# Optimization experiments

Measured on AMD Instinct MI355X. Metric: run time of the kernel, lower is better.

The kernel has to match this reference:

```python
import jax, jax.numpy as jnp
import numpy as np

B, C, H, W = 1, 96, 128, 128
P = 4            # patch_size
E = 192          # embed_dim
DI = 384         # d_inner = expand * embed_dim
NS = 16          # d_state
R = 12           # dt_rank = ceil(E/16)
K = 4            # scan directions
NBLK = 8         # SS2D_MBs_num
GW = C // 2      # SCPA group width


def layernorm(x, g, b, eps=1e-5):
    mu = x.mean(-1, keepdims=True)
    v = x.var(-1, keepdims=True)
    return (x - mu) * jax.lax.rsqrt(v + eps) * g + b


def batchnorm(x, g, b, m, v, eps=1e-5):
    # eval-mode BatchNorm2d over channel axis 1 of (B,C,H,W)
    return (x - m[:, None, None]) * jax.lax.rsqrt(v + eps)[:, None, None] * g[:, None, None] + b[:, None, None]


def conv2d(x, w):
    return jax.lax.conv_general_dilated(x, w, (1, 1), 'SAME', dimension_numbers=('NCHW', 'OIHW', 'NCHW'))


def dwconv2d(x, w, b):
    out = jax.lax.conv_general_dilated(x, w[:, None], (1, 1), 'SAME',
                                       dimension_numbers=('NCHW', 'OIHW', 'NCHW'),
                                       feature_group_count=w.shape[0])
    return out + b[None, :, None, None]


def lrelu(x):
    return jnp.where(x >= 0, x, 0.2 * x)


def channel_attention(x, w1, w2):
    # CBAM-style: shared MLP on avg+max pooled channel descriptors, sigmoid gate
    avg = x.mean((2, 3))
    mx = x.max((2, 3))
    mlp = lambda v: jax.nn.relu(v @ w1.T) @ w2.T
    attn = jax.nn.sigmoid(mlp(avg) + mlp(mx))
    return x * attn[:, :, None, None]


def selective_scan(xs, dts, A, Bs, Cs, Dskip):
    # xs,dts: (B,K,DI,L); A: (K,DI,NS); Bs,Cs: (B,K,NS,L); Dskip: (K,DI)
    xs_t = jnp.moveaxis(xs, -1, 0)
    dts_t = jnp.moveaxis(dts, -1, 0)
    Bs_t = jnp.moveaxis(Bs, -1, 0)
    Cs_t = jnp.moveaxis(Cs, -1, 0)
    h0 = jnp.zeros(xs.shape[:3] + (NS,), xs.dtype)  # (B,K,DI,NS)

    def step(h, t):
        xt, dt, Bt, Ct = t
        h = jnp.exp(dt[..., None] * A) * h + (dt * xt)[..., None] * Bt[:, :, None, :]
        return h, jnp.sum(h * Ct[:, :, None, :], axis=-1)

    _, ys = jax.lax.scan(step, h0, (xs_t, dts_t, Bs_t, Cs_t))
    return jnp.moveaxis(ys, 0, -1) + xs * Dskip[None, :, :, None]


def ss2d_block(x, p):
    # VMamba-style VSS block: x + SS2D(LN(x)); x: (B,Hp,Wp,E)
    (ln_g, ln_b, inproj_w, conv_w, conv_b, xproj_w, dtproj_w, dtproj_b,
     Alog, Dskip, on_g, on_b, outproj_w, merge_w) = p
    Bsz, Hp, Wp, _ = x.shape
    L = Hp * Wp
    h = layernorm(x, ln_g, ln_b)
    xz = jnp.einsum('bhwd,ed->bhwe', h, inproj_w)   # (B,Hp,Wp,2*DI)
    xc, z = jnp.split(xz, 2, axis=-1)
    xc = jax.nn.silu(dwconv2d(jnp.transpose(xc, (0, 3, 1, 2)), conv_w, conv_b))  # (B,DI,Hp,Wp)
    # 4-direction cross-scan: row-major, col-major and their reverses
    xf = xc.reshape(Bsz, DI, L)
    xwh = jnp.transpose(xc, (0, 1, 3, 2)).reshape(Bsz, DI, L)
    xs = jnp.stack([xf, xwh, jnp.flip(xf, -1), jnp.flip(xwh, -1)], axis=1)  # (B,K,DI,L)
    x_dbl = jnp.einsum('bkdl,kcd->bkcl', xs, xproj_w)  # (B,K,R+2*NS,L)
    dts, Bm, Cm = jnp.split(x_dbl, [R, R + NS], axis=2)
    dts = jax.nn.softplus(jnp.einsum('bkrl,kdr->bkdl', dts, dtproj_w) + dtproj_b[None, :, :, None])
    A = -jnp.exp(Alog)
    oy = selective_scan(xs, dts, A, Bm, Cm, Dskip)  # (B,K,DI,L)
    y0 = oy[:, 0]
    y1 = jnp.transpose(oy[:, 1].reshape(Bsz, DI, Wp, Hp), (0, 1, 3, 2)).reshape(Bsz, DI, L)
    y2 = jnp.flip(oy[:, 2], -1)
    y3 = jnp.transpose(jnp.flip(oy[:, 3], -1).reshape(Bsz, DI, Wp, Hp), (0, 1, 3, 2)).reshape(Bsz, DI, L)
    y = merge_w[0] * y0 + merge_w[1] * y1 + merge_w[2] * y2 + merge_w[3] * y3  # learnable merge
    y = jnp.transpose(y, (0, 2, 1)).reshape(Bsz, Hp, Wp, DI)
    y = layernorm(y, on_g, on_b) * jax.nn.silu(z)
    return x + jnp.einsum('bhwd,ed->bhwe', y, outproj_w)


def scpa(x, c1a, c1b, k1, k2w, k2b, k3, k4, c3):
    # PAN SCPA: two branches (3x3 conv / pixel-attention conv), 1x1 fuse, residual
    a = lrelu(jnp.einsum('bchw,oc->bohw', x, c1a))
    b = lrelu(jnp.einsum('bchw,oc->bohw', x, c1b))
    a = conv2d(a, k1)
    g = jax.nn.sigmoid(jnp.einsum('bchw,oc->bohw', b, k2w) + k2b[None, :, None, None])
    b = conv2d(conv2d(b, k3) * g, k4)
    out = jnp.einsum('bchw,oc->bohw', jnp.concatenate([lrelu(a), lrelu(b)], 1), c3)
    return out + x


def _forward(x, bn1_g, bn1_b, bn1_m, bn1_v, ca_w1, ca_w2, pe_w, pe_b, pu_w, pu_b,
             blk_ln_g, blk_ln_b, blk_inproj_w, blk_conv_w, blk_conv_b, blk_xproj_w,
             blk_dtproj_w, blk_dtproj_b, blk_Alog, blk_D, blk_on_g, blk_on_b,
             blk_outproj_w, blk_merge_w, bn2_g, bn2_b, bn2_m, bn2_v,
             scpa_c1a_w, scpa_c1b_w, scpa_k1_w, pa_k2_w, pa_k2_b, pa_k3_w, pa_k4_w, scpa_c3_w):
    residual = x
    h = batchnorm(x, bn1_g, bn1_b, bn1_m, bn1_v)
    x1 = channel_attention(h, ca_w1, ca_w2)
    Hp, Wp = H // P, W // P
    # patch embed: (B,C,H,W) -> (B,Hp,Wp,C*P*P) -> linear -> (B,Hp,Wp,E)
    xp = h.reshape(B, C, Hp, P, Wp, P).transpose(0, 2, 4, 1, 3, 5).reshape(B, Hp, Wp, C * P * P)
    x2 = xp @ pe_w.T + pe_b
    blk_params = (blk_ln_g, blk_ln_b, blk_inproj_w, blk_conv_w, blk_conv_b, blk_xproj_w,
                  blk_dtproj_w, blk_dtproj_b, blk_Alog, blk_D, blk_on_g, blk_on_b,
                  blk_outproj_w, blk_merge_w)
    x2, _ = jax.lax.scan(lambda c, p: (ss2d_block(c, p), None), x2, blk_params)
    # patch unembed
    xu = x2 @ pu_w.T + pu_b
    xu = xu.reshape(B, Hp, Wp, C, P, P).transpose(0, 3, 1, 4, 2, 5).reshape(B, C, H, W)
    xsum = residual + x1 + xu
    h2 = batchnorm(xsum, bn2_g, bn2_b, bn2_m, bn2_v)
    out = scpa(h2, scpa_c1a_w, scpa_c1b_w, scpa_k1_w, pa_k2_w, pa_k2_b, pa_k3_w, pa_k4_w, scpa_c3_w)
    return out + xsum


def setup_inputs():
    key = jax.random.key(0)
    kct = [0]
    def nk():
        kct[0] += 1
        return jax.random.fold_in(key, kct[0])
    def nrm(shape, s=0.02):
        return (jax.random.normal(nk(), shape) * s).astype(jnp.float32)
    f32 = jnp.float32
    inp = dict(
        x=jax.random.normal(nk(), (B, C, H, W), dtype=f32),
        bn1_g=jnp.ones((C,), f32), bn1_b=jnp.zeros((C,), f32),
        bn1_m=nrm((C,), 0.05), bn1_v=jnp.ones((C,), f32),
        ca_w1=nrm((C // 16, C), 0.1), ca_w2=nrm((C, C // 16), 0.1),
        pe_w=nrm((E, C * P * P)), pe_b=jnp.zeros((E,), f32),
        pu_w=nrm((C * P * P, E)), pu_b=jnp.zeros((C * P * P,), f32),
        blk_ln_g=jnp.ones((NBLK, E), f32), blk_ln_b=jnp.zeros((NBLK, E), f32),
        blk_inproj_w=nrm((NBLK, 2 * DI, E)),
        blk_conv_w=nrm((NBLK, DI, 3, 3), 0.1),
        blk_conv_b=jnp.zeros((NBLK, DI), f32),
        blk_xproj_w=nrm((NBLK, K, R + 2 * NS, DI)),
        blk_dtproj_w=nrm((NBLK, K, DI, R), 0.1),
        blk_dtproj_b=jnp.full((NBLK, K, DI), -4.6, f32),  # softplus ~= 0.01
        blk_Alog=jnp.broadcast_to(jnp.log(jnp.arange(1, NS + 1, dtype=f32)), (NBLK, K, DI, NS)) + 0.0,
        blk_D=jnp.ones((NBLK, K, DI), f32),
        blk_on_g=jnp.ones((NBLK, DI), f32), blk_on_b=jnp.zeros((NBLK, DI), f32),
        blk_outproj_w=nrm((NBLK, E, DI)),
        blk_merge_w=jnp.ones((NBLK, K), f32),
        bn2_g=jnp.ones((C,), f32), bn2_b=jnp.zeros((C,), f32),
        bn2_m=nrm((C,), 0.05), bn2_v=jnp.ones((C,), f32),
        scpa_c1a_w=nrm((GW, C), 0.05), scpa_c1b_w=nrm((GW, C), 0.05),
        scpa_k1_w=nrm((GW, GW, 3, 3), 0.05),
        pa_k2_w=nrm((GW, GW), 0.05), pa_k2_b=jnp.zeros((GW,), f32),
        pa_k3_w=nrm((GW, GW, 3, 3), 0.05), pa_k4_w=nrm((GW, GW, 3, 3), 0.05),
        scpa_c3_w=nrm((C, 2 * GW), 0.05),
    )
    return inp


def reference(x, bn1_g, bn1_b, bn1_m, bn1_v, ca_w1, ca_w2, pe_w, pe_b, pu_w, pu_b,
              blk_ln_g, blk_ln_b, blk_inproj_w, blk_conv_w, blk_conv_b, blk_xproj_w,
              blk_dtproj_w, blk_dtproj_b, blk_Alog, blk_D, blk_on_g, blk_on_b,
              blk_outproj_w, blk_merge_w, bn2_g, bn2_b, bn2_m, bn2_v,
              scpa_c1a_w, scpa_c1b_w, scpa_k1_w, pa_k2_w, pa_k2_b, pa_k3_w, pa_k4_w, scpa_c3_w):
    return _forward(x, bn1_g, bn1_b, bn1_m, bn1_v, ca_w1, ca_w2, pe_w, pe_b, pu_w, pu_b,
                    blk_ln_g, blk_ln_b, blk_inproj_w, blk_conv_w, blk_conv_b, blk_xproj_w,
                    blk_dtproj_w, blk_dtproj_b, blk_Alog, blk_D, blk_on_g, blk_on_b,
                    blk_outproj_w, blk_merge_w, bn2_g, bn2_b, bn2_m, bn2_v,
                    scpa_c1a_w, scpa_c1b_w, scpa_k1_w, pa_k2_w, pa_k2_b, pa_k3_w, pa_k4_w, scpa_c3_w)
```

## Files before the change

### kernel.cpp

```cpp
#include <hip/hip_runtime.h>
#include <math.h>

#define HW 16384
constexpr int C_ = 96;
constexpr int E_ = 192, DI_ = 384, NS_ = 16, R_ = 12, K_ = 4, NBLK_ = 8, GW_ = 48;
constexpr int L_ = 1024, CXP_ = 44;
constexpr int TC_ = 64;
constexpr int NCH_ = L_ / TC_;

__device__ __forceinline__ float lrelu_(float x){ return x >= 0.f ? x : 0.2f*x; }
__device__ __forceinline__ float sigmoid_(float x){ return 1.f/(1.f+expf(-x)); }
__device__ __forceinline__ float silu_(float x){ return x/(1.f+expf(-x)); }
__device__ __forceinline__ float softplus_(float x){ return fmaxf(x,0.f)+log1pf(expf(-fabsf(x))); }

__global__ void k_transAll(const float* __restrict__ peW, float* __restrict__ peWT,
                           const float* __restrict__ puW, float* __restrict__ puWT,
                           const float* __restrict__ inW, float* __restrict__ inWT,
                           const float* __restrict__ outW, float* __restrict__ outWT){
  __shared__ float t[32][33];
  int id = blockIdx.x;
  const float* in; float* out; int rows, cols, bx, by;
  if (id < 288){ in=peW; out=peWT; rows=192; cols=1536; bx=id%48; by=id/48; }
  else if (id < 576){ int r=id-288; in=puW; out=puWT; rows=1536; cols=192; bx=r%6; by=r/6; }
  else if (id < 1728){ int r=id-576; int z=r/144; int q=r%144;
    in=inW+(size_t)z*768*192; out=inWT+(size_t)z*768*192; rows=768; cols=192; bx=q%6; by=q/6; }
  else { int r=id-1728; int z=r/72; int q=r%72;
    in=outW+(size_t)z*192*384; out=outWT+(size_t)z*192*384; rows=192; cols=384; bx=q%12; by=q/12; }
  int r0=by*32, c0=bx*32, tx=threadIdx.x, ty=threadIdx.y;
  for (int i=0;i<32;i+=8){
    int r=r0+ty+i, c=c0+tx;
    if (r<rows && c<cols) t[ty+i][tx]=in[(size_t)r*cols+c];
  }
  __syncthreads();
  for (int i=0;i<32;i+=8){
    int c=c0+ty+i, r=r0+tx;
    if (r<rows && c<cols) out[(size_t)c*rows+r]=t[tx][ty+i];
  }
}

__global__ void k_bn1(const float* __restrict__ x, const float* g, const float* b,
                      const float* m, const float* v,
                      float* __restrict__ h, float* __restrict__ stats,
                      float* __restrict__ su, float* __restrict__ sq){
  int c = blockIdx.x, tid = threadIdx.x;
  int gid = c*256 + tid;
  if (gid < 1024){ su[gid] = 0.f; sq[gid] = 0.f; }
  float sc = g[c]*rsqrtf(v[c]+1e-5f), sh = b[c]-m[c]*sc;
  const float* xc = x + (size_t)c*HW;
  float* hc = h + (size_t)c*HW;
  float s = 0.f, mx = -1e30f;
  for (int i=tid;i<HW;i+=256){
    float val = fmaf(xc[i], sc, sh);
    hc[i] = val; s += val; mx = fmaxf(mx, val);
  }
  for (int o=32;o;o>>=1){ s += __shfl_xor(s,o); mx = fmaxf(mx, __shfl_xor(mx,o)); }
  __shared__ float ss[4], sm[4];
  int wid = tid>>6, lane = tid&63;
  if (!lane){ ss[wid]=s; sm[wid]=mx; }
  __syncthreads();
  if (!tid){
    stats[c] = (ss[0]+ss[1]+ss[2]+ss[3])*(1.f/HW);
    stats[96+c] = fmaxf(fmaxf(sm[0],sm[1]),fmaxf(sm[2],sm[3]));
  }
}

__global__ void k_attn(const float* __restrict__ stats, const float* __restrict__ w1,
                       const float* __restrict__ w2, float* __restrict__ attn){
  __shared__ float hid[12];
  int tid = threadIdx.x;
  if (tid < 12){
    int j = tid%6, which = tid/6;
    const float* vv = stats + which*96;
    float a = 0.f;
    for (int c=0;c<96;c++) a += vv[c]*w1[j*96+c];
    hid[tid] = fmaxf(a, 0.f);
  }
  __syncthreads();
  if (tid < 96){
    float a = 0.f;
    for (int j=0;j<6;j++) a += (hid[j]+hid[6+j])*w2[tid*6+j];
    attn[tid] = sigmoid_(a);
  }
}

__global__ __launch_bounds__(256) void k_gemmPE(const float* __restrict__ hsrc,
                      const float* __restrict__ wt, const float* __restrict__ bias,
                      float* __restrict__ out, float* __restrict__ su, float* __restrict__ sq){
  const int K = 1536, N = 192;
  __shared__ float As[32][34];
  __shared__ float Bs[32][32];
  int tid = threadIdx.x;
  int m0 = blockIdx.x*32, n0 = blockIdx.y*32;
  int tx = tid&15, ty = tid>>4;
  int arow = tid>>3, akq = tid&7;
  int brow = tid>>3, bn4 = tid&7;
  int m = m0+arow;
  int base2 = (m>>5)*512 + (m&31)*4;
  auto aload = [&](int kk)->float4 {
    int c = kk>>4, i2 = (kk>>2)&3;
    return *(const float4*)&hsrc[((size_t)c<<14) + (size_t)(i2*128 + base2)];
  };
  float4 aR = aload(akq*4);
  float4 bR = *(const float4*)&wt[(size_t)brow*N + n0 + bn4*4];
  float acc[2][2] = {{0}};
  for (int k0=0; k0<K; k0+=32){
    __syncthreads();
    As[akq*4+0][arow]=aR.x; As[akq*4+1][arow]=aR.y;
    As[akq*4+2][arow]=aR.z; As[akq*4+3][arow]=aR.w;
    *(float4*)&Bs[brow][bn4*4] = bR;
    __syncthreads();
    if (k0+32 < K){
      aR = aload(k0+32+akq*4);
      bR = *(const float4*)&wt[(size_t)(k0+32+brow)*N + n0 + bn4*4];
    }
    #pragma unroll
    for (int kk=0; kk<32; kk++){
      float2 av = *(const float2*)&As[kk][ty*2];
      float2 bv = *(const float2*)&Bs[kk][tx*2];
      acc[0][0] = fmaf(av.x, bv.x, acc[0][0]);
      acc[0][1] = fmaf(av.x, bv.y, acc[0][1]);
      acc[1][0] = fmaf(av.y, bv.x, acc[1][0]);
      acc[1][1] = fmaf(av.y, bv.y, acc[1][1]);
    }
  }
  float2 bq = *(const float2*)&bias[n0+tx*2];
  float sl[2], ql[2];
  #pragma unroll
  for (int i=0;i<2;i++){
    size_t o = (size_t)(m0+ty*2+i)*N + n0 + tx*2;
    float2 ov; ov.x = acc[i][0]+bq.x; ov.y = acc[i][1]+bq.y;
    *(float2*)&out[o] = ov;
    sl[i] = ov.x+ov.y; ql[i] = ov.x*ov.x+ov.y*ov.y;
  }
  #pragma unroll
  for (int o=8;o;o>>=1){
    sl[0]+=__shfl_xor(sl[0],o); ql[0]+=__shfl_xor(ql[0],o);
    sl[1]+=__shfl_xor(sl[1],o); ql[1]+=__shfl_xor(ql[1],o);
  }
  if (tx==0){
    atomicAdd(&su[m0+ty*2],   sl[0]); atomicAdd(&sq[m0+ty*2],   ql[0]);
    atomicAdd(&su[m0+ty*2+1], sl[1]); atomicAdd(&sq[m0+ty*2+1], ql[1]);
  }
}

__global__ __launch_bounds__(256) void k_gemm32s(const float* __restrict__ act,
                      const float* __restrict__ wt, const float* __restrict__ res,
                      float* __restrict__ out, float* __restrict__ su, float* __restrict__ sq,
                      int K, int N){
  __shared__ float As[32][34];
  __shared__ float Bs[32][32];
  int tid = threadIdx.x;
  int m0 = blockIdx.x*32, n0 = blockIdx.y*32;
  int tx = tid&15, ty = tid>>4;
  int arow = tid>>3, akq = tid&7;
  int brow = tid>>3, bn4 = tid&7;
  float4 aR = *(const float4*)&act[(size_t)(m0+arow)*K + akq*4];
  float4 bR = *(const float4*)&wt [(size_t)brow*N + n0 + bn4*4];
  float acc[2][2] = {{0}};
  for (int k0=0; k0<K; k0+=32){
    __syncthreads();
    As[akq*4+0][arow]=aR.x; As[akq*4+1][arow]=aR.y;
    As[akq*4+2][arow]=aR.z; As[akq*4+3][arow]=aR.w;
    *(float4*)&Bs[brow][bn4*4] = bR;
    __syncthreads();
    if (k0+32 < K){
      aR = *(const float4*)&act[(size_t)(m0+arow)*K + k0+32 + akq*4];
      bR = *(const float4*)&wt [(size_t)(k0+32+brow)*N + n0 + bn4*4];
    }
    #pragma unroll
    for (int kk=0; kk<32; kk++){
      float2 av = *(const float2*)&As[kk][ty*2];
      float2 bv = *(const float2*)&Bs[kk][tx*2];
      acc[0][0] = fmaf(av.x, bv.x, acc[0][0]);
      acc[0][1] = fmaf(av.x, bv.y, acc[0][1]);
      acc[1][0] = fmaf(av.y, bv.x, acc[1][0]);
      acc[1][1] = fmaf(av.y, bv.y, acc[1][1]);
    }
  }
  float sl[2], ql[2];
  #pragma unroll
  for (int i=0;i<2;i++){
    size_t o = (size_t)(m0+ty*2+i)*N + n0 + tx*2;
    float2 r = *(const float2*)&res[o];
    float2 ov; ov.x = acc[i][0]+r.x; ov.y = acc[i][1]+r.y;
    *(float2*)&out[o] = ov;
    sl[i] = ov.x+ov.y; ql[i] = ov.x*ov.x+ov.y*ov.y;
  }
  #pragma unroll
  for (int o=8;o;o>>=1){
    sl[0]+=__shfl_xor(sl[0],o); ql[0]+=__shfl_xor(ql[0],o);
    sl[1]+=__shfl_xor(sl[1],o); ql[1]+=__shfl_xor(ql[1],o);
  }
  if (tx==0){
    atomicAdd(&su[m0+ty*2],   sl[0]); atomicAdd(&sq[m0+ty*2],   ql[0]);
    atomicAdd(&su[m0+ty*2+1], sl[1]); atomicAdd(&sq[m0+ty*2+1], ql[1]);
  }
}

__global__ __launch_bounds__(256) void k_gemmPU(const float* __restrict__ act,
                      const float* __restrict__ wt, const float* __restrict__ bias,
                      float* __restrict__ out){
  const int K = 192, N = 1536;
  __shared__ float As[32][34];
  __shared__ float Bs[32][32];
  int tid = threadIdx.x;
  int m0 = blockIdx.x*32, n0 = blockIdx.y*32;
  int tx = tid&15, ty = tid>>4;
  int arow = tid>>3, akq = tid&7;
  int brow = tid>>3, bn4 = tid&7;
  float4 aR = *(const float4*)&act[(size_t)(m0+arow)*K + akq*4];
  float4 bR = *(const float4*)&wt [(size_t)brow*N + n0 + bn4*4];
  float acc[2][2] = {{0}};
  for (int k0=0; k0<K; k0+=32){
    __syncthreads();
    As[akq*4+0][arow]=aR.x; As[akq*4+1][arow]=aR.y;
    As[akq*4+2][arow]=aR.z; As[akq*4+3][arow]=aR.w;
    *(float4*)&Bs[brow][bn4*4] = bR;
    __syncthreads();
    if (k0+32 < K){
      aR = *(const float4*)&act[(size_t)(m0+arow)*K + k0+32 + akq*4];
      bR = *(const float4*)&wt [(size_t)(k0+32+brow)*N + n0 + bn4*4];
    }
    #pragma unroll
    for (int kk=0; kk<32; kk++){
      float2 av = *(const float2*)&As[kk][ty*2];
      float2 bv = *(const float2*)&Bs[kk][tx*2];
      acc[0][0] = fmaf(av.x, bv.x, acc[0][0]);
      acc[0][1] = fmaf(av.x, bv.y, acc[0][1]);
      acc[1][0] = fmaf(av.y, bv.x, acc[1][0]);
      acc[1][1] = fmaf(av.y, bv.y, acc[1][1]);
    }
  }
  int n = n0 + tx*2;
  float2 bq = *(const float2*)&bias[n];
  int c = n>>4, i2 = (n>>2)&3, j = n&3;
  #pragma unroll
  for (int i=0;i<2;i++){
    int m = m0+ty*2+i;
    size_t o = ((size_t)c<<14) + (size_t)((m>>5)*4+i2)*128 + (m&31)*4 + j;
    float2 ov; ov.x = acc[i][0]+bq.x; ov.y = acc[i][1]+bq.y;
    *(float2*)&out[o] = ov;
  }
}

__global__ __launch_bounds__(256) void k_gemm32ln(const float* __restrict__ act,
                      const float* __restrict__ wt, const float* __restrict__ lg,
                      const float* __restrict__ lb, const float* __restrict__ su,
                      const float* __restrict__ sq, float* __restrict__ out,
                      int K, int N){
  __shared__ float As[32][34];
  __shared__ float Bs[32][32];
  int tid = threadIdx.x;
  int m0 = blockIdx.x*32, n0 = blockIdx.y*32;
  int tx = tid&15, ty = tid>>4;
  int arow = tid>>3, akq = tid&7;
  int brow = tid>>3, bn4 = tid&7;
  float m = su[m0+arow]*(1.f/192.f);
  float r = rsqrtf(sq[m0+arow]*(1.f/192.f) - m*m + 1e-5f);
  float4 aR = *(const float4*)&act[(size_t)(m0+arow)*K + akq*4];
  float4 gR = *(const float4*)&lg[akq*4];
  float4 hR = *(const float4*)&lb[akq*4];
  float4 bR = *(const float4*)&wt[(size_t)brow*N + n0 + bn4*4];
  float acc[2][2] = {{0}};
  for (int k0=0; k0<K; k0+=32){
    __syncthreads();
    As[akq*4+0][arow] = (aR.x-m)*r*gR.x + hR.x;
    As[akq*4+1][arow] = (aR.y-m)*r*gR.y + hR.y;
    As[akq*4+2][arow] = (aR.z-m)*r*gR.z + hR.z;
    As[akq*4+3][arow] = (aR.w-m)*r*gR.w + hR.w;
    *(float4*)&Bs[brow][bn4*4] = bR;
    __syncthreads();
    if (k0+32 < K){
      aR = *(const float4*)&act[(size_t)(m0+arow)*K + k0+32 + akq*4];
      gR = *(const float4*)&lg[k0+32+akq*4];
      hR = *(const float4*)&lb[k0+32+akq*4];
      bR = *(const float4*)&wt[(size_t)(k0+32+brow)*N + n0 + bn4*4];
    }
    #pragma unroll
    for (int kk=0; kk<32; kk++){
      float2 av = *(const float2*)&As[kk][ty*2];
      float2 bv = *(const float2*)&Bs[kk][tx*2];
      acc[0][0] = fmaf(av.x, bv.x, acc[0][0]);
      acc[0][1] = fmaf(av.x, bv.y, acc[0][1]);
      acc[1][0] = fmaf(av.y, bv.x, acc[1][0]);
      acc[1][1] = fmaf(av.y, bv.y, acc[1][1]);
    }
  }
  #pragma unroll
  for (int i=0;i<2;i++){
    size_t o = (size_t)(m0+ty*2+i)*N + n0 + tx*2;
    float2 ov; ov.x = acc[i][0]; ov.y = acc[i][1];
    *(float2*)&out[o] = ov;
  }
}

__global__ __launch_bounds__(256) void k_dwxst(const float* __restrict__ xz,
                        const float* __restrict__ w, const float* __restrict__ bias,
                        float* __restrict__ xcs, float* __restrict__ xst0,
                        float* __restrict__ xst1){
  __shared__ float ld[96][33];
  __shared__ float t[32][33];
  int h0 = blockIdx.x;
  int d0 = blockIdx.y*32;
  int tx = threadIdx.x, ty = threadIdx.y;
  #pragma unroll
  for (int i=0;i<12;i++){
    int ll = i*8 + ty;
    int h = h0 - 1 + (ll>>5);
    int wv = ll & 31;
    float v = 0.f;
    if ((unsigned)h < 32u) v = xz[(size_t)(h*32+wv)*768 + d0 + tx];
    ld[ll][tx] = v;
  }
  __syncthreads();
  #pragma unroll
  for (int i=0;i<4;i++){
    int dl = ty + 8*i;
    int d = d0 + dl;
    float acc = bias[d];
    const float* wp = w + d*9;
    #pragma unroll
    for (int di=0;di<3;di++){
      #pragma unroll
      for (int dj=0;dj<3;dj++){
        int wq = tx + dj - 1;
        if ((unsigned)wq < 32u)
          acc = fmaf(ld[di*32 + wq][dl], wp[di*3+dj], acc);
      }
    }
    float val = silu_(acc);
    xcs[(size_t)d*L_ + h0*32 + tx] = val;
    t[dl][tx] = val;
  }
  __syncthreads();
  int d = d0 + tx;
  #pragma unroll
  for (int i=0;i<4;i++){
    int wq = ty + 8*i;
    int l = h0*32 + wq;
    float val = t[tx][wq];
    int t1 = wq*32 + h0;
    xst0[(size_t)l*DI_ + d] = val;
    xst1[(size_t)t1*DI_ + d] = val;
  }
}

__global__ __launch_bounds__(256) void k_xdblP(const float* __restrict__ xcs,
                       const float* __restrict__ xw, float* __restrict__ xdblP){
  int kz = blockIdx.z;
  int k = kz & 3, sp = kz >> 2;
  int s = blockIdx.x*256 + threadIdx.x;
  int Ts = ((s&31)<<5) | (s>>5);
  int lw;
  if (k==0) lw = s;
  else if (k==1) lw = Ts;
  else if (k==2) lw = 1023-s;
  else lw = 1023-Ts;
  int c0 = blockIdx.y*4;
  const float* wp = xw + ((size_t)k*CXP_ + c0)*DI_ + sp*128;
  const float* src = xcs + s + (size_t)sp*128*L_;
  float a0=0,a1=0,a2=0,a3=0;
  for (int d=0; d<128; d++){
    float v = src[(size_t)d*L_];
    a0 = fmaf(v, wp[d],        a0);
    a1 = fmaf(v, wp[DI_+d],    a1);
    a2 = fmaf(v, wp[2*DI_+d],  a2);
    a3 = fmaf(v, wp[3*DI_+d],  a3);
  }
  size_t base = (((size_t)sp*4 + k)*CXP_ + c0)*L_ + lw;
  xdblP[base]       = a0;
  xdblP[base+L_]    = a1;
  xdblP[base+2*L_]  = a2;
  xdblP[base+3*L_]  = a3;
}

__global__ void k_dtbc(const float* __restrict__ xdblP, const float* __restrict__ dtw,
                       const float* __restrict__ dtb, float* __restrict__ dts_t,
                       float* __restrict__ bc){
  int k = blockIdx.y, l = blockIdx.x, d = threadIdx.x;
  const float* p0 = xdblP + ((size_t)(0+k)*CXP_)*L_ + l;
  const float* p1 = xdblP + ((size_t)(4+k)*CXP_)*L_ + l;
  const float* p2 = xdblP + ((size_t)(8+k)*CXP_)*L_ + l;
  float acc = dtb[(size_t)k*DI_ + d];
  const float* w = dtw + ((size_t)k*DI_ + d)*R_;
  #pragma unroll
  for (int r=0;r<R_;r++){
    size_t o = (size_t)r*L_;
    acc = fmaf(p0[o]+p1[o]+p2[o], w[r], acc);
  }
  dts_t[((size_t)k*L_ + l)*DI_ + d] = softplus_(acc);
  if (d < 32){
    size_t o = (size_t)(R_+d)*L_;
    bc[((size_t)k*L_ + l)*32 + d] = p0[o]+p1[o]+p2[o];
  }
}

__global__ __launch_bounds__(256) void k_scanA(const float* __restrict__ xst0,
                      const float* __restrict__ xst1,
                      const float* __restrict__ dts_t, const float* __restrict__ bc,
                      const float* __restrict__ Alog,
                      float* __restrict__ Ech, float* __restrict__ Hch){
  int k = blockIdx.z;
  int d = blockIdx.y*16 + (threadIdx.x>>4);
  int n = threadIdx.x&15;
  int ch = blockIdx.x;
  float A = -expf(Alog[((size_t)k*DI_ + d)*NS_ + n]);
  float aL2 = A * 1.4426950408889634f;
  int t0 = ch*TC_;
  const float* dtp = dts_t + ((size_t)k*L_ + t0)*DI_ + d;
  const float* bcp = bc    + ((size_t)k*L_ + t0)*32;
  const float* xb = (k&1) ? xst1 : xst0;
  const float* xp_; ptrdiff_t xs_;
  if (k < 2){ xp_ = xb + (size_t)t0*DI_ + d; xs_ = DI_; }
  else      { xp_ = xb + (size_t)(1023-t0)*DI_ + d; xs_ = -(ptrdiff_t)DI_; }
  float h = 0.f, Ep = 1.f;
  #pragma unroll 4
  for (int t=0;t<TC_;t++){
    float dt = dtp[(size_t)t*DI_];
    float xv = xp_[(ptrdiff_t)t*xs_];
    float Bn = bcp[t*32+n];
    float e = exp2f(aL2*dt);
    h = fmaf(e, h, dt*xv*Bn);
    Ep *= e;
  }
  size_t idx = (((size_t)k*NCH_ + ch)*DI_ + d)*NS_ + n;
  Ech[idx] = Ep; Hch[idx] = h;
}

__global__ void k_scanB(const float* __restrict__ Ech, const float* __restrict__ Hch,
                        float* __restrict__ carry){
  int idx = blockIdx.x*256 + threadIdx.x;
  int k = idx / (DI_*NS_);
  int dn = idx % (DI_*NS_);
  float h = 0.f;
  #pragma unroll
  for (int c=0;c<NCH_;c++){
    size_t o = ((size_t)(k*NCH_+c)*DI_*NS_) + dn;
    carry[o] = h;
    h = fmaf(Ech[o], h, Hch[o]);
  }
}

__global__ __launch_bounds__(256) void k_scanC(const float* __restrict__ xst0,
                      const float* __restrict__ xst1,
                      const float* __restrict__ dts_t, const float* __restrict__ bc,
                      const float* __restrict__ Alog, const float* __restrict__ carry,
                      float* __restrict__ yst){
  int k = blockIdx.z;
  int d = blockIdx.y*16 + (threadIdx.x>>4);
  int n = threadIdx.x&15;
  int ch = blockIdx.x;
  float A = -expf(Alog[((size_t)k*DI_ + d)*NS_ + n]);
  float aL2 = A * 1.4426950408889634f;
  int t0 = ch*TC_;
  const float* dtp = dts_t + ((size_t)k*L_ + t0)*DI_ + d;
  const float* bcp = bc    + ((size_t)k*L_ + t0)*32;
  const float* xb = (k&1) ? xst1 : xst0;
  const float* xp_; ptrdiff_t xs_;
  if (k < 2){ xp_ = xb + (size_t)t0*DI_ + d; xs_ = DI_; }
  else      { xp_ = xb + (size_t)(1023-t0)*DI_ + d; xs_ = -(ptrdiff_t)DI_; }
  float* yp = yst + ((size_t)k*L_ + t0)*DI_ + d;
  float h = carry[(((size_t)k*NCH_ + ch)*DI_ + d)*NS_ + n];
  #pragma unroll 4
  for (int t=0;t<TC_;t++){
    float dt = dtp[(size_t)t*DI_];
    float xv = xp_[(ptrdiff_t)t*xs_];
    float Bn = bcp[t*32+n], Cn = bcp[t*32+16+n];
    float e = exp2f(aL2*dt);
    h = fmaf(e, h, dt*xv*Bn);
    float p = h*Cn;
    p += __shfl_xor(p,1); p += __shfl_xor(p,2);
    p += __shfl_xor(p,4); p += __shfl_xor(p,8);
    if (n==0) yp[(size_t)t*DI_] = p;
  }
}

__global__ void k_merge(const float* __restrict__ yst, const float* __restrict__ xst0,
                        const float* __restrict__ xst1,
                        const float* __restrict__ Dsk, const float* __restrict__ mw,
                        const float* __restrict__ ong, const float* __restrict__ onb,
                        const float* __restrict__ xz, float* __restrict__ out,
                        float* __restrict__ su, float* __restrict__ sq){
  int l = blockIdx.x, d = threadIdx.x;
  if (d == 0){ su[l] = 0.f; sq[l] = 0.f; }
  int T = ((l&31)<<5) | (l>>5);
  int tt[4] = { l, T, 1023-l, 1023-T };
  float xv0 = xst0[(size_t)l*DI_ + d];
  float xv1 = xst1[(size_t)T*DI_ + d];
  float v = 0.f;
  #pragma unroll
  for (int k=0;k<4;k++){
    float xk = (k&1) ? xv1 : xv0;
    v += mw[k]*(yst[(size_t)(k*L_ + tt[k])*DI_ + d] + xk*Dsk[k*DI_+d]);
  }
  float s = v, sqv = v*v;
  for (int o=32;o;o>>=1){ s += __shfl_xor(s,o); sqv += __shfl_xor(sqv,o); }
  __shared__ float rs_[6], rq_[6];
  int lane = d&63, wid = d>>6;
  if (!lane){ rs_[wid]=s; rq_[wid]=sqv; }
  __syncthreads();
  float ts=0.f, tq=0.f;
  #pragma unroll
  for (int i=0;i<6;i++){ ts += rs_[i]; tq += rq_[i]; }
  float mu = ts*(1.f/DI_);
  float rstd = rsqrtf(tq*(1.f/DI_) - mu*mu + 1e-5f);
  float y = (v-mu)*rstd*ong[d] + onb[d];
  float z = xz[(size_t)l*768 + DI_ + d];
  out[(size_t)l*DI_ + d] = y * silu_(z);
}

__global__ void k_sum(const float* __restrict__ x, const float* __restrict__ h,
                      const float* __restrict__ attn, const float* __restrict__ xu,
                      const float* g2, const float* b2, const float* m2, const float* v2,
                      float* __restrict__ xsum, float* __restrict__ h2){
  int idx = blockIdx.x*256 + threadIdx.x;
  int c = idx>>14;
  float s = x[idx] + h[idx]*attn[c] + xu[idx];
  xsum[idx] = s;
  h2[idx] = (s - m2[c])*rsqrtf(v2[c]+1e-5f)*g2[c] + b2[c];
}

__global__ __launch_bounds__(256) void k_1x1ab(const float* __restrict__ h2,
                        const float* __restrict__ wa, const float* __restrict__ wb,
                        float* __restrict__ a, float* __restrict__ b){
  __shared__ float lw[96*12];
  int ocg = blockIdx.x;
  for (int i=threadIdx.x; i<96*12; i+=256){
    int o = i%12, c = i/12;
    lw[i] = (o<6) ? wa[(ocg*6 + o)*96 + c] : wb[(ocg*6 + (o-6))*96 + c];
  }
  __syncthreads();
  int p = blockIdx.y*256 + threadIdx.x;
  float acc[12];
  #pragma unroll
  for (int o=0;o<12;o++) acc[o]=0.f;
  for (int c=0;c<96;c++){
    float v = h2[(size_t)c*HW + p];
    const float* w = lw + c*12;
    #pragma unroll
    for (int o=0;o<12;o++) acc[o] = fmaf(v, w[o], acc[o]);
  }
  #pragma unroll
  for (int o=0;o<6;o++){
    a[(size_t)(ocg*6+o)*HW + p] = lrelu_(acc[o]);
    b[(size_t)(ocg*6+o)*HW + p] = lrelu_(acc[6+o]);
  }
}

__global__ __launch_bounds__(256) void k_1x1g(const float* __restrict__ b,
                       const float* __restrict__ w, const float* __restrict__ bias,
                       float* __restrict__ g){
  __shared__ float lw[48*6];
  int ocg = blockIdx.x;
  for (int i=threadIdx.x; i<48*6; i+=256){
    int o = i%6, c = i/6;
    lw[i] = w[(ocg*6 + o)*48 + c];
  }
  __syncthreads();
  int p = blockIdx.y*256 + threadIdx.x;
  float acc[6];
  #pragma unroll
  for (int o=0;o<6;o++) acc[o] = bias[ocg*6+o];
  for (int c=0;c<48;c++){
    float v = b[(size_t)c*HW + p];
    const float* wp = lw + c*6;
    #pragma unroll
    for (int o=0;o<6;o++) acc[o] = fmaf(v, wp[o], acc[o]);
  }
  #pragma unroll
  for (int o=0;o<6;o++) g[(size_t)(ocg*6+o)*HW + p] = sigmoid_(acc[o]);
}

__global__ __launch_bounds__(256) void k_conv3d(const float* __restrict__ inA,
                        const float* __restrict__ wA, const float* __restrict__ inB,
                        const float* __restrict__ wB, const float* __restrict__ aux,
                        float* __restrict__ outA, float* __restrict__ outB){
  __shared__ float lw[48*9*6];
  __shared__ float ld[8][4][130];
  int half = blockIdx.x >> 3;
  int ocg = blockIdx.x & 7;
  const float* in = half ? inB : inA;
  const float* w  = half ? wB : wA;
  int tid = threadIdx.x;
  for (int i=tid; i<48*9*6; i+=256){
    int o = i%6, j = (i/6)%9, ic = i/54;
    lw[i] = w[((size_t)(ocg*6+o)*48 + ic)*9 + j];
  }
  if (tid < 32){ ld[tid>>2][tid&3][0] = 0.f; ld[tid>>2][tid&3][129] = 0.f; }
  int p = blockIdx.y*256 + tid;
  int ww = p&127;
  int hbase = blockIdx.y*2 - 1;
  int lr = 1 + (tid>>7);
  float acc[6];
  #pragma unroll
  for (int o=0;o<6;o++) acc[o]=0.f;
  for (int ic0=0; ic0<48; ic0+=8){
    __syncthreads();
    #pragma unroll
    for (int q=0;q<16;q++){
      int i = tid + q*256;
      int icl = i>>9, rem = i&511;
      int r = rem>>7, cp = rem&127;
      int gy = hbase + r;
      ld[icl][r][cp+1] = ((unsigned)gy < 128u) ? in[(size_t)(ic0+icl)*HW + gy*128 + cp] : 0.f;
    }
    __syncthreads();
    #pragma unroll
    for (int icl=0; icl<8; icl++){
      const float* lwp = lw + (ic0+icl)*54;
      #pragma unroll
      for (int di=0;di<3;di++){
        #pragma unroll
        for (int dj=0;dj<3;dj++){
          float xv = ld[icl][lr-1+di][ww+dj];
          const float* wj = lwp + (di*3+dj)*6;
          #pragma unroll
          for (int o=0;o<6;o++) acc[o] = fmaf(xv, wj[o], acc[o]);
        }
      }
    }
  }
  if (half == 0){
    #pragma unroll
    for (int o=0;o<6;o++)
      outA[(size_t)(ocg*6+o)*HW + p] = lrelu_(acc[o]);
  } else {
    #pragma unroll
    for (int o=0;o<6;o++){
      size_t oi = (size_t)(ocg*6+o)*HW + p;
      outB[oi] = acc[o]*aux[oi];
    }
  }
}

__global__ __launch_bounds__(256) void k_conv3(const float* __restrict__ in,
                        const float* __restrict__ w, float* __restrict__ out){
  __shared__ float lw[48*9*6];
  __shared__ float ld[8][4][130];
  int ocg = blockIdx.x;
  int tid = threadIdx.x;
  for (int i=tid; i<48*9*6; i+=256){
    int o = i%6, j = (i/6)%9, ic = i/54;
    lw[i] = w[((size_t)(ocg*6+o)*48 + ic)*9 + j];
  }
  if (tid < 32){ ld[tid>>2][tid&3][0] = 0.f; ld[tid>>2][tid&3][129] = 0.f; }
  int p = blockIdx.y*256 + tid;
  int ww = p&127;
  int hbase = blockIdx.y*2 - 1;
  int lr = 1 + (tid>>7);
  float acc[6];
  #pragma unroll
  for (int o=0;o<6;o++) acc[o]=0.f;
  for (int ic0=0; ic0<48; ic0+=8){
    __syncthreads();
    #pragma unroll
    for (int q=0;q<16;q++){
      int i = tid + q*256;
      int icl = i>>9, rem = i&511;
      int r = rem>>7, cp = rem&127;
      int gy = hbase + r;
      ld[icl][r][cp+1] = ((unsigned)gy < 128u) ? in[(size_t)(ic0+icl)*HW + gy*128 + cp] : 0.f;
    }
    __syncthreads();
    #pragma unroll
    for (int icl=0; icl<8; icl++){
      const float* lwp = lw + (ic0+icl)*54;
      #pragma unroll
      for (int di=0;di<3;di++){
        #pragma unroll
        for (int dj=0;dj<3;dj++){
          float xv = ld[icl][lr-1+di][ww+dj];
          const float* wj = lwp + (di*3+dj)*6;
          #pragma unroll
          for (int o=0;o<6;o++) acc[o] = fmaf(xv, wj[o], acc[o]);
        }
      }
    }
  }
  #pragma unroll
  for (int o=0;o<6;o++)
    out[(size_t)(ocg*6+o)*HW + p] = lrelu_(acc[o]);
}

__global__ __launch_bounds__(256) void k_c3(const float* __restrict__ ab,
                     const float* __restrict__ w, const float* __restrict__ h2,
                     const float* __restrict__ xsum, float* __restrict__ out){
  __shared__ float lw[96*12];
  int ocg = blockIdx.x;
  for (int i=threadIdx.x; i<96*12; i+=256){
    int o = i%12, j = i/12;
    lw[i] = w[(ocg*12 + o)*96 + j];
  }
  __syncthreads();
  int p = blockIdx.y*256 + threadIdx.x;
  float acc[12];
  #pragma unroll
  for (int o=0;o<12;o++) acc[o]=0.f;
  for (int j=0;j<96;j++){
    float v = ab[(size_t)j*HW + p];
    const float* wp = lw + j*12;
    #pragma unroll
    for (int o=0;o<12;o++) acc[o] = fmaf(v, wp[o], acc[o]);
  }
  #pragma unroll
  for (int o=0;o<12;o++){
    size_t oi = (size_t)(ocg*12+o)*HW + p;
    out[oi] = acc[o] + h2[oi] + xsum[oi];
  }
}

extern "C" void kernel_launch(void* const* d_in, const int* in_sizes, int n_in,
                              void* d_out, int out_size, void* d_ws, size_t ws_size,
                              hipStream_t stream){
  (void)in_sizes; (void)n_in; (void)out_size; (void)ws_size;
  const float* x    = (const float*)d_in[0];
  const float* bn1g = (const float*)d_in[1];
  const float* bn1b = (const float*)d_in[2];
  const float* bn1m = (const float*)d_in[3];
  const float* bn1v = (const float*)d_in[4];
  const float* caw1 = (const float*)d_in[5];
  const float* caw2 = (const float*)d_in[6];
  const float* peW  = (const float*)d_in[7];
  const float* peb  = (const float*)d_in[8];
  const float* puW  = (const float*)d_in[9];
  const float* pub  = (const float*)d_in[10];
  const float* lng  = (const float*)d_in[11];
  const float* lnb  = (const float*)d_in[12];
  const float* inW  = (const float*)d_in[13];
  const float* convw= (const float*)d_in[14];
  const float* convb= (const float*)d_in[15];
  const float* xprojw=(const float*)d_in[16];
  const float* dtw  = (const float*)d_in[17];
  const float* dtb  = (const float*)d_in[18];
  const float* Alog = (const float*)d_in[19];
  const float* Dsk  = (const float*)d_in[20];
  const float* ong  = (const float*)d_in[21];
  const float* onb  = (const float*)d_in[22];
  const float* outW = (const float*)d_in[23];
  const float* mw   = (const float*)d_in[24];
  const float* bn2g = (const float*)d_in[25];
  const float* bn2b = (const float*)d_in[26];
  const float* bn2m = (const float*)d_in[27];
  const float* bn2v = (const float*)d_in[28];
  const float* c1a  = (const float*)d_in[29];
  const float* c1b  = (const float*)d_in[30];
  const float* k1w  = (const float*)d_in[31];
  const float* k2w  = (const float*)d_in[32];
  const float* k2b  = (const float*)d_in[33];
  const float* k3w  = (const float*)d_in[34];
  const float* k4w  = (const float*)d_in[35];
  const float* c3w  = (const float*)d_in[36];
  float* out = (float*)d_out;

  float* ws = (float*)d_ws;
  size_t off = 0;
  auto alloc = [&](size_t n){ float* p = ws + off; off += n; return p; };
  float* peWT  = alloc((size_t)1536*192);
  float* puWT  = alloc((size_t)192*1536);
  float* inWT  = alloc((size_t)8*192*768);
  float* outWT = alloc((size_t)8*384*192);
  float* bufH  = alloc((size_t)96*HW);
  float* stats = alloc(256);
  float* attn  = alloc(128);
  float* bufP  = alloc((size_t)1024*1536);
  float* x2a   = alloc((size_t)1024*192);
  float* x2b   = alloc((size_t)1024*192);
  float* bufXZ = alloc((size_t)1024*768);
  float* bufXCS= alloc((size_t)384*1024);
  float* bufXST= alloc((size_t)4*1024*384);
  float* xdblP = alloc((size_t)12*44*1024);
  float* dts   = alloc((size_t)4*1024*384);
  float* bc    = alloc((size_t)4*1024*32);
  float* yst   = alloc((size_t)4*1024*384);
  float* bufY  = alloc((size_t)1024*384);
  float* xsum  = alloc((size_t)96*HW);
  float* h2    = alloc((size_t)96*HW);
  float* Ech   = alloc((size_t)K_*NCH_*DI_*NS_);
  float* Hch   = alloc((size_t)K_*NCH_*DI_*NS_);
  float* carry = alloc((size_t)K_*NCH_*DI_*NS_);
  float* suB   = alloc(1024);
  float* sqB   = alloc(1024);
  float* xst0  = bufXST;
  float* xst1  = bufXST + (size_t)L_*DI_;

  dim3 tb(32,8);
  k_transAll<<<2304, tb, 0, stream>>>(peW, peWT, puW, puWT, inW, inWT, outW, outWT);

  k_bn1<<<96,256,0,stream>>>(x, bn1g, bn1b, bn1m, bn1v, bufH, stats, suB, sqB);
  k_attn<<<1,128,0,stream>>>(stats, caw1, caw2, attn);
  k_gemmPE<<<dim3(32,6),256,0,stream>>>(bufH, peWT, peb, x2a, suB, sqB);

  float* cur = x2a; float* nxt = x2b;
  for (int b=0;b<8;b++){
    k_gemm32ln<<<dim3(32,24),256,0,stream>>>(cur, inWT+(size_t)b*192*768,
                        lng+(size_t)b*192, lnb+(size_t)b*192, suB, sqB, bufXZ, 192, 768);
    k_dwxst<<<dim3(32,12),tb,0,stream>>>(bufXZ, convw+(size_t)b*384*9,
                        convb+(size_t)b*384, bufXCS, xst0, xst1);
    k_xdblP<<<dim3(4,11,12),256,0,stream>>>(bufXCS, xprojw+(size_t)b*4*44*384, xdblP);
    k_dtbc<<<dim3(1024,4),384,0,stream>>>(xdblP, dtw+(size_t)b*4*384*12, dtb+(size_t)b*4*384, dts, bc);
    const float* Ab = Alog + (size_t)b*4*384*16;
    k_scanA<<<dim3(NCH_,DI_/16,4),256,0,stream>>>(xst0, xst1, dts, bc, Ab, Ech, Hch);
    k_scanB<<<(K_*DI_*NS_)/256,256,0,stream>>>(Ech, Hch, carry);
    k_scanC<<<dim3(NCH_,DI_/16,4),256,0,stream>>>(xst0, xst1, dts, bc, Ab, carry, yst);
    k_merge<<<1024,384,0,stream>>>(yst, xst0, xst1, Dsk+(size_t)b*4*384, mw+(size_t)b*4,
                                   ong+(size_t)b*384, onb+(size_t)b*384, bufXZ, bufY, suB, sqB);
    k_gemm32s<<<dim3(32,6),256,0,stream>>>(bufY, outWT+(size_t)b*384*192, cur, nxt, suB, sqB, 384, 192);
    float* t = cur; cur = nxt; nxt = t;
  }

  k_gemmPU<<<dim3(32,48),256,0,stream>>>(cur, puWT, pub, bufP);
  k_sum<<<(96*HW)/256,256,0,stream>>>(x, bufH, attn, bufP, bn2g, bn2b, bn2m, bn2v, xsum, h2);

  float* bufA = dts;
  float* bufB = dts + (size_t)48*HW;
  float* bufG = yst;
  float* bufT = yst + (size_t)48*HW;
  float* ab   = bufXST;
  k_1x1ab<<<dim3(8,64),256,0,stream>>>(h2, c1a, c1b, bufA, bufB);
  k_1x1g<<<dim3(8,64),256,0,stream>>>(bufB, k2w, k2b, bufG);
  k_conv3d<<<dim3(16,64),256,0,stream>>>(bufA, k1w, bufB, k3w, bufG, ab, bufT);
  k_conv3<<<dim3(8,64),256,0,stream>>>(bufT, k4w, ab+(size_t)48*HW);
  k_c3<<<dim3(8,64),256,0,stream>>>(ab, c3w, h2, xsum, out);
}
```

Baseline: 1.121 ms.

## Fold scan carry propagation into scanC and swap SCPA grid axes

The separate k_scanB launch that turned per-chunk decay and state into carries is removed. Each k_scanC thread now recomputes its incoming carry by folding over all earlier chunks' Ech and Hch values before its own chunk, which saves one launch and the carry buffer per block. The cost is redundant serial work of up to 15 steps per thread. The SCPA convolution kernels also swap grid dimensions so spatial tiles lie along x and channel groups along y, which changes block scheduling order and cache locality.

```diff
diff --git a/kernel.cpp b/kernel.cpp
--- a/kernel.cpp
+++ b/kernel.cpp
@@ -427,24 +427,11 @@
   Ech[idx] = Ep; Hch[idx] = h;
 }
 
-__global__ void k_scanB(const float* __restrict__ Ech, const float* __restrict__ Hch,
-                        float* __restrict__ carry){
-  int idx = blockIdx.x*256 + threadIdx.x;
-  int k = idx / (DI_*NS_);
-  int dn = idx % (DI_*NS_);
-  float h = 0.f;
-  #pragma unroll
-  for (int c=0;c<NCH_;c++){
-    size_t o = ((size_t)(k*NCH_+c)*DI_*NS_) + dn;
-    carry[o] = h;
-    h = fmaf(Ech[o], h, Hch[o]);
-  }
-}
-
 __global__ __launch_bounds__(256) void k_scanC(const float* __restrict__ xst0,
                       const float* __restrict__ xst1,
                       const float* __restrict__ dts_t, const float* __restrict__ bc,
-                      const float* __restrict__ Alog, const float* __restrict__ carry,
+                      const float* __restrict__ Alog,
+                      const float* __restrict__ Ech, const float* __restrict__ Hch,
                       float* __restrict__ yst){
   int k = blockIdx.z;
   int d = blockIdx.y*16 + (threadIdx.x>>4);
@@ -460,7 +447,13 @@
   if (k < 2){ xp_ = xb + (size_t)t0*DI_ + d; xs_ = DI_; }
   else      { xp_ = xb + (size_t)(1023-t0)*DI_ + d; xs_ = -(ptrdiff_t)DI_; }
   float* yp = yst + ((size_t)k*L_ + t0)*DI_ + d;
-  float h = carry[(((size_t)k*NCH_ + ch)*DI_ + d)*NS_ + n];
+  float h = 0.f;
+  size_t dn = ((size_t)k*NCH_*DI_ + d)*0;
+  for (int c=0;c<ch;c++){
+    size_t o = (((size_t)k*NCH_ + c)*DI_ + d)*NS_ + n;
+    h = fmaf(Ech[o], h, Hch[o]);
+  }
+  (void)dn;
   #pragma unroll 4
   for (int t=0;t<TC_;t++){
     float dt = dtp[(size_t)t*DI_];
@@ -524,13 +517,13 @@
                         const float* __restrict__ wa, const float* __restrict__ wb,
                         float* __restrict__ a, float* __restrict__ b){
   __shared__ float lw[96*12];
-  int ocg = blockIdx.x;
+  int ocg = blockIdx.y;
   for (int i=threadIdx.x; i<96*12; i+=256){
     int o = i%12, c = i/12;
     lw[i] = (o<6) ? wa[(ocg*6 + o)*96 + c] : wb[(ocg*6 + (o-6))*96 + c];
   }
   __syncthreads();
-  int p = blockIdx.y*256 + threadIdx.x;
+  int p = blockIdx.x*256 + threadIdx.x;
   float acc[12];
   #pragma unroll
   for (int o=0;o<12;o++) acc[o]=0.f;
@@ -551,13 +544,13 @@
                        const float* __restrict__ w, const float* __restrict__ bias,
                        float* __restrict__ g){
   __shared__ float lw[48*6];
-  int ocg = blockIdx.x;
+  int ocg = blockIdx.y;
   for (int i=threadIdx.x; i<48*6; i+=256){
     int o = i%6, c = i/6;
     lw[i] = w[(ocg*6 + o)*48 + c];
   }
   __syncthreads();
-  int p = blockIdx.y*256 + threadIdx.x;
+  int p = blockIdx.x*256 + threadIdx.x;
   float acc[6];
   #pragma unroll
   for (int o=0;o<6;o++) acc[o] = bias[ocg*6+o];
@@ -577,8 +570,9 @@
                         float* __restrict__ outA, float* __restrict__ outB){
   __shared__ float lw[48*9*6];
   __shared__ float ld[8][4][130];
-  int half = blockIdx.x >> 3;
-  int ocg = blockIdx.x & 7;
+  int sp = blockIdx.x;
+  int half = blockIdx.y >> 3;
+  int ocg = blockIdx.y & 7;
   const float* in = half ? inB : inA;
   const float* w  = half ? wB : wA;
   int tid = threadIdx.x;
@@ -587,9 +581,9 @@
     lw[i] = w[((size_t)(ocg*6+o)*48 + ic)*9 + j];
   }
   if (tid < 32){ ld[tid>>2][tid&3][0] = 0.f; ld[tid>>2][tid&3][129] = 0.f; }
-  int p = blockIdx.y*256 + tid;
+  int p = sp*256 + tid;
   int ww = p&127;
-  int hbase = blockIdx.y*2 - 1;
+  int hbase = sp*2 - 1;
   int lr = 1 + (tid>>7);
   float acc[6];
   #pragma unroll
@@ -637,16 +631,17 @@
                         const float* __restrict__ w, float* __restrict__ out){
   __shared__ float lw[48*9*6];
   __shared__ float ld[8][4][130];
-  int ocg = blockIdx.x;
+  int sp = blockIdx.x;
+  int ocg = blockIdx.y;
   int tid = threadIdx.x;
   for (int i=tid; i<48*9*6; i+=256){
     int o = i%6, j = (i/6)%9, ic = i/54;
     lw[i] = w[((size_t)(ocg*6+o)*48 + ic)*9 + j];
   }
   if (tid < 32){ ld[tid>>2][tid&3][0] = 0.f; ld[tid>>2][tid&3][129] = 0.f; }
-  int p = blockIdx.y*256 + tid;
+  int p = sp*256 + tid;
   int ww = p&127;
-  int hbase = blockIdx.y*2 - 1;
+  int hbase = sp*2 - 1;
   int lr = 1 + (tid>>7);
   float acc[6];
   #pragma unroll
@@ -686,13 +681,13 @@
                      const float* __restrict__ w, const float* __restrict__ h2,
                      const float* __restrict__ xsum, float* __restrict__ out){
   __shared__ float lw[96*12];
-  int ocg = blockIdx.x;
+  int ocg = blockIdx.y;
   for (int i=threadIdx.x; i<96*12; i+=256){
     int o = i%12, j = i/12;
     lw[i] = w[(ocg*12 + o)*96 + j];
   }
   __syncthreads();
-  int p = blockIdx.y*256 + threadIdx.x;
+  int p = blockIdx.x*256 + threadIdx.x;
   float acc[12];
   #pragma unroll
   for (int o=0;o<12;o++) acc[o]=0.f;
@@ -777,7 +772,6 @@
   float* h2    = alloc((size_t)96*HW);
   float* Ech   = alloc((size_t)K_*NCH_*DI_*NS_);
   float* Hch   = alloc((size_t)K_*NCH_*DI_*NS_);
-  float* carry = alloc((size_t)K_*NCH_*DI_*NS_);
   float* suB   = alloc(1024);
   float* sqB   = alloc(1024);
   float* xst0  = bufXST;
@@ -800,8 +794,7 @@
     k_dtbc<<<dim3(1024,4),384,0,stream>>>(xdblP, dtw+(size_t)b*4*384*12, dtb+(size_t)b*4*384, dts, bc);
     const float* Ab = Alog + (size_t)b*4*384*16;
     k_scanA<<<dim3(NCH_,DI_/16,4),256,0,stream>>>(xst0, xst1, dts, bc, Ab, Ech, Hch);
-    k_scanB<<<(K_*DI_*NS_)/256,256,0,stream>>>(Ech, Hch, carry);
-    k_scanC<<<dim3(NCH_,DI_/16,4),256,0,stream>>>(xst0, xst1, dts, bc, Ab, carry, yst);
+    k_scanC<<<dim3(NCH_,DI_/16,4),256,0,stream>>>(xst0, xst1, dts, bc, Ab, Ech, Hch, yst);
     k_merge<<<1024,384,0,stream>>>(yst, xst0, xst1, Dsk+(size_t)b*4*384, mw+(size_t)b*4,
                                    ong+(size_t)b*384, onb+(size_t)b*384, bufXZ, bufY, suB, sqB);
     k_gemm32s<<<dim3(32,6),256,0,stream>>>(bufY, outWT+(size_t)b*384*192, cur, nxt, suB, sqB, 384, 192);
@@ -816,9 +809,9 @@
   float* bufG = yst;
   float* bufT = yst + (size_t)48*HW;
   float* ab   = bufXST;
-  k_1x1ab<<<dim3(8,64),256,0,stream>>>(h2, c1a, c1b, bufA, bufB);
-  k_1x1g<<<dim3(8,64),256,0,stream>>>(bufB, k2w, k2b, bufG);
-  k_conv3d<<<dim3(16,64),256,0,stream>>>(bufA, k1w, bufB, k3w, bufG, ab, bufT);
-  k_conv3<<<dim3(8,64),256,0,stream>>>(bufT, k4w, ab+(size_t)48*HW);
-  k_c3<<<dim3(8,64),256,0,stream>>>(ab, c3w, h2, xsum, out);
-}
+  k_1x1ab<<<dim3(64,8),256,0,stream>>>(h2, c1a, c1b, bufA, bufB);
+  k_1x1g<<<dim3(64,8),256,0,stream>>>(bufB, k2w, k2b, bufG);
+  k_conv3d<<<dim3(64,16),256,0,stream>>>(bufA, k1w, bufB, k3w, bufG, ab, bufT);
+  k_conv3<<<dim3(64,8),256,0,stream>>>(bufT, k4w, ab+(size_t)48*HW);
+  k_c3<<<dim3(64,8),256,0,stream>>>(ab, c3w, h2, xsum, out);
+}
```

Result: slower. 1.204 ms (+7.3%).
